# Kernel optimization log

Hardware: AMD Instinct MI355X
Metric: run time of the kernel (lower is better)

The kernel has to match this reference:

```python
import jax, jax.numpy as jnp
import numpy as np

B, N, H, F = 4, 256, 192, 64
SUP = 1.0  # ancestor_suppression_strength
EPS = 1e-6


def setup_inputs() -> dict:
    key = jax.random.key(0)
    ks = jax.random.split(key, 14)
    z = jax.random.normal(ks[0], (B, H), jnp.float32)
    # strictly-lower-triangular 0/1 parent (link) matrix: row t lists parents j < t
    tri = jnp.tril(jnp.ones((N, N), jnp.float32), -1)
    targets = (jax.random.uniform(ks[1], (B, N, N)) < 0.05).astype(jnp.float32) * tri

    def w(k, shape):
        fan_in = shape[0]
        return jax.random.normal(k, shape, jnp.float32) / jnp.sqrt(jnp.float32(fan_in))

    return {
        "z": z,
        "teacher_forcing_targets": targets,
        "W_init": w(ks[2], (H, H)), "b_init": jnp.zeros((H,), jnp.float32),
        "W_ih": w(ks[3], (H, 3 * H)), "W_hh": w(ks[4], (H, 3 * H)),
        "b_ih": jnp.zeros((3 * H,), jnp.float32), "b_hh": jnp.zeros((3 * H,), jnp.float32),
        "W1": w(ks[5], (3 * H, H)), "b1": jnp.zeros((H,), jnp.float32),
        "W2": w(ks[6], (H, 1)), "b2": jnp.zeros((1,), jnp.float32),
        "Wf": w(ks[7], (H, F)), "bf": jnp.zeros((F,), jnp.float32),
        "atom_count": N,
    }


def gru_cell(x, h, W_ih, W_hh, b_ih, b_hh):
    gx = x @ W_ih + b_ih
    gh = h @ W_hh + b_hh
    xr, xu, xn = jnp.split(gx, 3, axis=-1)
    hr, hu, hn = jnp.split(gh, 3, axis=-1)
    r = jax.nn.sigmoid(xr + hr)
    u = jax.nn.sigmoid(xu + hu)
    n = jnp.tanh(xn + r * hn)
    return (1.0 - u) * n + u * h


def reference(z, teacher_forcing_targets, W_init, b_init, W_ih, W_hh, b_ih, b_hh,
              W1, b1, W2, b2, Wf, bf, atom_count):
    b, n = teacher_forcing_targets.shape[0], teacher_forcing_targets.shape[1]
    h = z.shape[-1]
    idx = jnp.arange(n)

    # decoder_init: latent z -> hidden state of node 0
    h0 = jnp.tanh(z @ W_init + b_init)
    S0 = jnp.zeros((b, n, h), z.dtype).at[:, 0].set(h0)   # node states
    A0 = jnp.zeros((b, n, n), z.dtype)                    # ancestor indicator A[b,i,j]=1 iff j ancestor of i

    def step(carry, xs):
        S, A, ll = carry
        t, tgt = xs                                   # t scalar, tgt (B,N) = parents of node t
        mask = (idx < t).astype(S.dtype)              # existing nodes
        cnt = jnp.maximum(mask.sum(), 1.0)
        # mean-aggregation over existing node states -> GRU message
        m = (S * mask[None, :, None]).sum(axis=1) / cnt              # (B,H)
        h_prov = gru_cell(m, z, W_ih, W_hh, b_ih, b_hh)              # provisional state of new node
        # parent logits: MLP([h_new, h_existing, z]) per candidate parent
        feats = jnp.concatenate([
            jnp.broadcast_to(h_prov[:, None, :], S.shape), S,
            jnp.broadcast_to(z[:, None, :], S.shape)], axis=-1)      # (B,N,3H)
        logits = (jax.nn.relu(feats @ W1 + b1) @ W2 + b2)[..., 0]    # (B,N)
        # ancestor suppression: suppress j if j is already an ancestor of one of t's parents
        reach = jnp.einsum('bn,bnm->bm', tgt, A)
        anc = (reach > 0).astype(S.dtype)
        p = jax.nn.sigmoid(logits) * (1.0 - SUP * anc)
        p = jnp.clip(p, EPS, 1.0 - EPS)
        ll = ll + (mask[None, :] * (tgt * jnp.log(p) + (1.0 - tgt) * jnp.log1p(-p))).sum()
        # teacher forcing: commit parents, update new-node state from parent states
        deg = jnp.maximum(tgt.sum(axis=-1, keepdims=True), 1.0)
        msg = jnp.einsum('bn,bnh->bh', tgt, S) / deg
        h_new = gru_cell(msg, h_prov, W_ih, W_hh, b_ih, b_hh)
        S = jax.lax.dynamic_update_slice(S, h_new[:, None, :], (0, t, 0))
        row = jnp.minimum(tgt + anc, 1.0)             # ancestors(t) = parents U ancestors(parents)
        A = jax.lax.dynamic_update_slice(A, row[:, None, :], (0, t, 0))
        return (S, A, ll), None

    ts = jnp.arange(1, n)
    tgt_rows = jnp.swapaxes(teacher_forcing_targets[:, 1:, :], 0, 1)  # (N-1,B,N)
    (S, A, ll), _ = jax.lax.scan(step, (S0, A0, jnp.zeros((), z.dtype)), (ts, tgt_rows))

    L = teacher_forcing_targets            # teacher-forced link matrix
    node_features = S @ Wf + bf            # node_feature_decoder head
    return L, node_features, ll
```

## Files before the change

kernel.cpp:

```cpp
#include <hip/hip_runtime.h>
#include <stdint.h>

#define B_ 4
#define N_ 256
#define H_ 192
#define H3_ 576
#define F_ 64

#define H0_OFF   0u
#define ZC_OFF   1024u
#define HL_OFF   2048u
#define SL_OFF   395264u
#define AN_OFF   788480u
#define TG_OFF   796672u
#define PL_OFF   804864u
#define PC_OFF   870400u
#define DG_OFF   871424u
#define D_OFF    872448u
#define G_OFF    1462272u
#define C_OFF    1658880u
#define FHL_OFF  1855488u
#define FSL_OFF  2248704u
#define XC_OFF   2641920u

#define AN64 (AN_OFF/2)
#define TG64 (TG_OFF/2)

#define NF_OUT 262144u
#define LL_OUT 327680u

__device__ __forceinline__ float sigm_(float x){ return 1.0f/(1.0f + __expf(-x)); }
__device__ __forceinline__ float tanh_(float x){
  float ax = fabsf(x);
  float e = __expf(-2.0f*ax);
  float t = (1.0f - e)/(1.0f + e);
  return x < 0.0f ? -t : t;
}

__device__ __forceinline__ void st_mall_(uint32_t* p, unsigned long long u){
  __hip_atomic_store((unsigned long long*)p, u, __ATOMIC_RELAXED, __HIP_MEMORY_SCOPE_AGENT);
}
__device__ __forceinline__ unsigned long long ld_mall_(const uint32_t* p){
  return __hip_atomic_load((const unsigned long long*)p, __ATOMIC_RELAXED, __HIP_MEMORY_SCOPE_AGENT);
}
__device__ __forceinline__ unsigned long long ld_l2_(const uint32_t* p){
  unsigned long long v;
  asm volatile("buffer_inv sc0\n\t"
               "s_waitcnt vmcnt(0)\n\t"
               "global_load_dwordx2 %0, %1, off\n\t"
               "s_waitcnt vmcnt(0)"
               : "=v"(v) : "v"(p) : "memory");
  return v;
}
__device__ __forceinline__ void pub_(uint32_t* fp, uint32_t* mp, float v, uint32_t tag){
  unsigned long long u = ((unsigned long long)tag<<32) | (unsigned long long)__float_as_uint(v);
  __hip_atomic_store((unsigned long long*)fp, u, __ATOMIC_RELAXED, __HIP_MEMORY_SCOPE_WORKGROUP);
  st_mall_(mp, u);
}
__device__ __forceinline__ float pollH_(const uint32_t* fp, const uint32_t* mp, int fast, uint32_t tag){
  unsigned long long x = 0; int it = 0;
  for(;;){
    if (fast){
      x = ld_l2_(fp);
      if ((uint32_t)(x>>32) != tag && (((++it) & 3) == 3)){
        unsigned long long m = ld_mall_(mp);
        if ((uint32_t)(m>>32) == tag) x = m;
      }
    } else {
      x = ld_mall_(mp);
    }
    if (__all((int)((uint32_t)(x>>32) == tag))) break;
  }
  return __uint_as_float((uint32_t)x);
}

__global__ void __launch_bounds__(192) k_pre1(const float* __restrict__ z,
    const float* __restrict__ Winit, const float* __restrict__ binit,
    const float* __restrict__ W1, const float* __restrict__ b1,
    const float* __restrict__ tgt, float* ws, float* out)
{
  int bx = blockIdx.x, b = blockIdx.y, tid = threadIdx.x;
  if (bx == N_){
    __shared__ float zs[H_];
    zs[tid] = z[b*H_ + tid];
    __syncthreads();
    float a0=0.f, a1=0.f;
    for (int k=0;k<H_;k++){
      float zv = zs[k];
      a0 += zv * Winit[(size_t)k*H_ + tid];
      a1 += zv * W1[(size_t)(2*H_ + k)*H_ + tid];
    }
    ws[H0_OFF + b*H_ + tid] = tanh_(a0 + binit[tid]);
    ws[ZC_OFF + b*H_ + tid] = a1 + b1[tid];
    if (b==0 && tid==0) out[LL_OUT] = 0.0f;
    return;
  }
  if (tid >= 64) return;
  int t = bx, lane = tid;
  uint32_t* wsu = (uint32_t*)ws;
  unsigned long long* ws64 = (unsigned long long*)ws;
  const float* row = tgt + ((size_t)(b*N_) + t)*N_;
  uint8_t* pl = ((uint8_t*)&wsu[PL_OFF]) + (size_t)(b*N_ + t)*N_;
  int cnt = 0;
  #pragma unroll
  for (int m=0;m<4;m++){
    float v = row[m*64 + lane];
    bool p = (v != 0.0f);
    unsigned long long bw = __ballot(p);
    if (lane == 0) ws64[TG64 + (size_t)(b*N_+t)*4 + m] = bw;
    if (p){
      int pos = cnt + (int)__popcll(bw & ((1ULL<<lane)-1ULL));
      pl[pos] = (uint8_t)(m*64 + lane);
    }
    cnt += (int)__popcll(bw);
  }
  if (lane == 0){
    wsu[PC_OFF + b*N_ + t] = (uint32_t)cnt;
    ws[DG_OFF + b*N_ + t] = 1.0f / fmaxf((float)cnt, 1.0f);
  }
}

__global__ void __launch_bounds__(512, 2) k_pass1(const float* __restrict__ z,
    const float* __restrict__ Wih, const float* __restrict__ Whh,
    const float* __restrict__ bih_g, const float* __restrict__ bhh_g,
    float* ws)
{
  int bx = blockIdx.x;
  int b = bx & 7;
  if (b >= B_) return;
  int blk = bx >> 3;
  int tid = threadIdx.x;
  const int e  = tid >> 3;
  const int kc = tid & 7;
  const int E  = blk*64 + e;

  float* wsf = ws;
  uint32_t* wsu = (uint32_t*)ws;
  unsigned long long* ws64 = (unsigned long long*)ws;

  __shared__ __align__(16) float sh[H_];
  __shared__ __align__(16) float ss[H_];
  __shared__ float sDG[N_], sTF1[N_];
  __shared__ uint32_t sPC[N_];
  __shared__ int sfast[4];
  __shared__ unsigned long long sAB[N_][4];

  {
    float v = wsf[H0_OFF + b*H_ + E];
    if (kc == 0)
      pub_(&wsu[FSL_OFF + (unsigned)(b*N_)*384u + 2u*(unsigned)E],
           &wsu[SL_OFF  + (unsigned)(b*N_)*384u + 2u*(unsigned)E], v, 1u);
    if (kc == 1) ss[E] = v;
  }

  uint32_t xcc = (uint32_t)__builtin_amdgcn_s_getreg((31u<<11) | 20u) & 15u;
  if (tid == 0)
    __hip_atomic_store(&wsu[XC_OFF + b*16 + blk], 0xC0DE0000u | xcc,
                       __ATOMIC_RELAXED, __HIP_MEMORY_SCOPE_AGENT);
  if (tid < 64){
    uint32_t v = 0; int ok;
    do {
      v = (tid < 3) ? __hip_atomic_load(&wsu[XC_OFF + b*16 + tid],
              __ATOMIC_RELAXED, __HIP_MEMORY_SCOPE_AGENT) : (0xC0DE0000u | xcc);
      ok = (int)((v >> 16) == 0xC0DEu);
    } while (!__all(ok));
    if (tid < 3) sfast[tid] = ((v & 0xFFu) == xcc) ? 1 : 0;
  }

  for (int i = tid; i < N_; i += 512){
    sDG[i] = wsf[DG_OFF + b*N_ + i];
    sPC[i] = wsu[PC_OFF + b*N_ + i];
    float f1 = 0.f;
    if (i >= 1){
      unsigned long long w1 = ws64[TG64 + (size_t)(b*N_+i)*4 + ((i-1)>>6)];
      f1 = (float)((w1 >> ((i-1)&63)) & 1ULL);
    }
    sTF1[i] = f1;
  }
  if (blk == 0 && tid >= 192 && tid < 196) sAB[0][tid-192] = 0ULL;

  float rwih[3][24], rwhh[3][24], rbih[3], rbhh[3], rghz[3];
  #pragma unroll
  for (int g=0; g<3; g++){
    int col = g*H_ + E;
    #pragma unroll
    for (int i=0;i<24;i++){
      rwih[g][i] = Wih[(size_t)(kc*24+i)*H3_ + col];
      rwhh[g][i] = Whh[(size_t)(kc*24+i)*H3_ + col];
    }
    rbih[g] = bih_g[col];
    rbhh[g] = bhh_g[col];
  }
  {
    float a0=0.f,a1=0.f,a2=0.f;
    #pragma unroll
    for (int i=0;i<24;i++){
      float zv = z[b*H_ + kc*24 + i];
      a0 += zv*rwhh[0][i]; a1 += zv*rwhh[1][i]; a2 += zv*rwhh[2][i];
    }
    #pragma unroll
    for (int m=1;m<8;m<<=1){
      a0 += __shfl_xor(a0,m); a1 += __shfl_xor(a1,m); a2 += __shfl_xor(a2,m);
    }
    rghz[0]=a0+rbhh[0]; rghz[1]=a1+rbhh[1]; rghz[2]=a2+rbhh[2];
  }
  float zreg = z[b*H_ + E];

  __syncthreads();
  if (tid < 128){
    int j = (tid < blk*64) ? tid : tid + 64;
    ss[j] = pollH_(&wsu[FSL_OFF + (unsigned)(b*N_)*384u + 2u*(unsigned)j],
                   &wsu[SL_OFF  + (unsigned)(b*N_)*384u + 2u*(unsigned)j],
                   sfast[j>>6], 1u);
  }
  __syncthreads();

  float q0=0.f, q1=0.f, q2=0.f;
  const uint8_t* plbase = ((const uint8_t*)&wsu[PL_OFF]) + (size_t)(b*N_)*N_;
  float* Dbase = wsf + D_OFF + (size_t)((b*3+blk)*N_)*H_;

  for (int t=1; t<N_; t++){
    const uint32_t tagH = (uint32_t)(t+1);
    float d0=0.f,d1=0.f,d2=0.f;
    #pragma unroll
    for (int c=0;c<6;c++){
      float4 v4 = *(const float4*)&ss[kc*24 + c*4];
      float xx0=v4.x, xx1=v4.y, xx2=v4.z, xx3=v4.w;
      d0 += xx0*rwih[0][c*4+0]; d1 += xx0*rwih[1][c*4+0]; d2 += xx0*rwih[2][c*4+0];
      d0 += xx1*rwih[0][c*4+1]; d1 += xx1*rwih[1][c*4+1]; d2 += xx1*rwih[2][c*4+1];
      d0 += xx2*rwih[0][c*4+2]; d1 += xx2*rwih[1][c*4+2]; d2 += xx2*rwih[2][c*4+2];
      d0 += xx3*rwih[0][c*4+3]; d1 += xx3*rwih[1][c*4+3]; d2 += xx3*rwih[2][c*4+3];
    }
    #pragma unroll
    for (int m=1;m<8;m<<=1){
      d0 += __shfl_xor(d0,m); d1 += __shfl_xor(d1,m); d2 += __shfl_xor(d2,m);
    }
    q0 += d0; q1 += d1; q2 += d2;
    float invt = 1.0f/(float)t;
    float r = sigm_(q0*invt + rbih[0] + rghz[0]);
    float u = sigm_(q1*invt + rbih[1] + rghz[1]);
    float n = tanh_(q2*invt + rbih[2] + r*rghz[2]);
    float hp = (1.0f-u)*n + u*zreg;
    if (kc == 0){
      pub_(&wsu[FHL_OFF + (unsigned)(b*N_+t)*384u + 2u*(unsigned)E],
           &wsu[HL_OFF  + (unsigned)(b*N_+t)*384u + 2u*(unsigned)E], hp, tagH);
      float* Dr = Dbase + (size_t)(t-1)*H_;
      Dr[e] = d0; Dr[64+e] = d1; Dr[128+e] = d2;
    }
    if (kc == 1) sh[E] = hp;
    float ga0=0.f, ga1=0.f, ga2=0.f;
    {
      int pc = (int)sPC[t];
      const uint8_t* pl = plbase + (size_t)t*N_;
      for (int i=kc; i<pc; i+=8){
        int p = pl[i];
        if (p == t-1) continue;
        const float* Dp = Dbase + (size_t)p*H_;
        ga0 += Dp[e]; ga1 += Dp[64+e]; ga2 += Dp[128+e];
      }
    }
    #pragma unroll
    for (int m=1;m<8;m<<=1){
      ga0 += __shfl_xor(ga0,m); ga1 += __shfl_xor(ga1,m); ga2 += __shfl_xor(ga2,m);
    }
    if (tid < 128){
      int j = (tid < blk*64) ? tid : tid + 64;
      sh[j] = pollH_(&wsu[FHL_OFF + (unsigned)(b*N_+t)*384u + 2u*(unsigned)j],
                     &wsu[HL_OFF  + (unsigned)(b*N_+t)*384u + 2u*(unsigned)j],
                     sfast[j>>6], tagH);
    } else if (blk == 0 && tid >= 192 && tid < 208){
      int lane16 = tid - 192;
      int ip = lane16 >> 2, w = lane16 & 3;
      int pc = (int)sPC[t];
      const uint8_t* pl = plbase + (size_t)t*N_;
      unsigned long long acc = 0ULL;
      for (int i=ip; i<pc; i+=4) acc |= sAB[pl[i]][w];
      acc |= __shfl_xor(acc, 4);
      acc |= __shfl_xor(acc, 8);
      if (ip == 0){
        ws64[AN64 + (size_t)(b*N_+t)*4 + w] = acc;
        sAB[t][w] = acc | ws64[TG64 + (size_t)(b*N_+t)*4 + w];
      }
    }
    __syncthreads();
    float y0=0.f,y1=0.f,y2=0.f;
    #pragma unroll
    for (int c=0;c<6;c++){
      float4 v4 = *(const float4*)&sh[kc*24 + c*4];
      float xx0=v4.x, xx1=v4.y, xx2=v4.z, xx3=v4.w;
      y0 += xx0*rwhh[0][c*4+0]; y1 += xx0*rwhh[1][c*4+0]; y2 += xx0*rwhh[2][c*4+0];
      y0 += xx1*rwhh[0][c*4+1]; y1 += xx1*rwhh[1][c*4+1]; y2 += xx1*rwhh[2][c*4+1];
      y0 += xx2*rwhh[0][c*4+2]; y1 += xx2*rwhh[1][c*4+2]; y2 += xx2*rwhh[2][c*4+2];
      y0 += xx3*rwhh[0][c*4+3]; y1 += xx3*rwhh[1][c*4+3]; y2 += xx3*rwhh[2][c*4+3];
    }
    #pragma unroll
    for (int m=1;m<8;m<<=1){
      y0 += __shfl_xor(y0,m); y1 += __shfl_xor(y1,m); y2 += __shfl_xor(y2,m);
    }
    float dginv = sDG[t], tf1 = sTF1[t];
    float gxa = (ga0 + tf1*d0)*dginv + rbih[0];
    float gxb = (ga1 + tf1*d1)*dginv + rbih[1];
    float gxc = (ga2 + tf1*d2)*dginv + rbih[2];
    float r2 = sigm_(gxa + y0 + rbhh[0]);
    float u2 = sigm_(gxb + y1 + rbhh[1]);
    float n2 = tanh_(gxc + r2*(y2 + rbhh[2]));
    float hn = (1.0f-u2)*n2 + u2*hp;
    if (kc == 0)
      pub_(&wsu[FSL_OFF + (unsigned)(b*N_+t)*384u + 2u*(unsigned)E],
           &wsu[SL_OFF  + (unsigned)(b*N_+t)*384u + 2u*(unsigned)E], hn, tagH);
    if (kc == 1) ss[E] = hn;
    if (tid < 128){
      int j = (tid < blk*64) ? tid : tid + 64;
      ss[j] = pollH_(&wsu[FSL_OFF + (unsigned)(b*N_+t)*384u + 2u*(unsigned)j],
                     &wsu[SL_OFF  + (unsigned)(b*N_+t)*384u + 2u*(unsigned)j],
                     sfast[j>>6], tagH);
    }
    __syncthreads();
  }
}

__global__ void k_p2a(const float* __restrict__ W1, const float* __restrict__ Wf,
    const float* __restrict__ bf, float* ws, float* out)
{
  int j = blockIdx.x, b = blockIdx.y, tid = threadIdx.x;
  __shared__ float srow[H_], hrow[H_];
  __shared__ float nfp[3][F_];
  srow[tid] = ws[SL_OFF + (unsigned)(b*N_+j)*384u + 2u*tid];
  hrow[tid] = ws[HL_OFF + (unsigned)(b*N_+j)*384u + 2u*tid];
  __syncthreads();
  float accG = 0.f, accC = 0.f;
  for (int k=0;k<H_;k++){
    float sv = srow[k], hv = hrow[k];
    accG += sv * W1[(size_t)(H_+k)*H_ + tid];
    accC += hv * W1[(size_t)k*H_ + tid];
  }
  ws[G_OFF + ((size_t)b*H_ + tid)*N_ + j] = accG;
  ws[C_OFF + (size_t)(b*N_+j)*H_ + tid] = accC + ws[ZC_OFF + b*H_ + tid];
  int f = tid & 63, kp = tid >> 6;
  float a = 0.f;
  for (int i=0;i<64;i++){ int k = kp*64 + i; a += srow[k]*Wf[(size_t)k*F_ + f]; }
  nfp[kp][f] = a;
  __syncthreads();
  if (tid < F_) out[NF_OUT + (size_t)(b*N_+j)*F_ + tid] = nfp[0][tid]+nfp[1][tid]+nfp[2][tid] + bf[tid];
}

__global__ void __launch_bounds__(256) k_p2b(const float* __restrict__ W2,
    const float* __restrict__ b2p, float* ws, float* out)
{
  int t = blockIdx.x + 1, b = blockIdx.y;
  int tid = threadIdx.x; int lane = tid & 63; int wv = tid >> 6;
  __shared__ float cv[H_], w2s[H_];
  __shared__ float wsum[4];
  unsigned long long* ws64 = (unsigned long long*)ws;
  if (tid < H_){
    cv[tid] = ws[C_OFF + (size_t)(b*N_+t)*H_ + tid];
    w2s[tid] = W2[tid];
  }
  __syncthreads();
  float acc = 0.f;
  if (tid < t){
    const float* GT = ws + G_OFF + (size_t)b*H_*N_;
    float a = 0.f;
    for (int k=0;k<H_;k++) a += fmaxf(cv[k] + GT[(size_t)k*N_ + tid], 0.f) * w2s[k];
    float logit = a + b2p[0];
    float pp = 1.0f/(1.0f+__expf(-logit));
    unsigned long long an = ws64[AN64 + (size_t)(b*N_+t)*4 + (tid>>6)];
    unsigned long long tg = ws64[TG64 + (size_t)(b*N_+t)*4 + (tid>>6)];
    float anc = (float)((an >> (tid&63)) & 1ULL);
    pp = pp * (1.0f - anc);
    pp = fminf(fmaxf(pp, 1e-6f), 1.0f - 1e-6f);
    int tgb = (int)((tg >> (tid&63)) & 1ULL);
    acc = tgb ? logf(pp) : log1pf(-pp);
  }
  #pragma unroll
  for (int m=32;m>=1;m>>=1) acc += __shfl_xor(acc, m);
  if (lane == 0) wsum[wv] = acc;
  __syncthreads();
  if (tid == 0) atomicAdd(out + LL_OUT, wsum[0]+wsum[1]+wsum[2]+wsum[3]);
}

extern "C" void kernel_launch(void* const* d_in, const int* in_sizes, int n_in,
                              void* d_out, int out_size, void* d_ws, size_t ws_size,
                              hipStream_t stream) {
  (void)in_sizes; (void)n_in; (void)out_size; (void)ws_size;
  const float* z     = (const float*)d_in[0];
  const float* tgt   = (const float*)d_in[1];
  const float* Winit = (const float*)d_in[2];
  const float* binit = (const float*)d_in[3];
  const float* Wih   = (const float*)d_in[4];
  const float* Whh   = (const float*)d_in[5];
  const float* bih   = (const float*)d_in[6];
  const float* bhh   = (const float*)d_in[7];
  const float* W1    = (const float*)d_in[8];
  const float* b1    = (const float*)d_in[9];
  const float* W2    = (const float*)d_in[10];
  const float* b2    = (const float*)d_in[11];
  const float* Wf    = (const float*)d_in[12];
  const float* bf    = (const float*)d_in[13];
  float* out = (float*)d_out;
  float* ws  = (float*)d_ws;

  hipMemcpyAsync(d_out, d_in[1], (size_t)B_*N_*N_*sizeof(float), hipMemcpyDeviceToDevice, stream);

  k_pre1<<<dim3(N_+1, B_), dim3(192), 0, stream>>>(z, Winit, binit, W1, b1, tgt, ws, out);
  k_pass1<<<dim3(24), dim3(512), 0, stream>>>(z, Wih, Whh, bih, bhh, ws);
  k_p2a<<<dim3(N_, B_), dim3(H_), 0, stream>>>(W1, Wf, bf, ws, out);
  k_p2b<<<dim3(N_-1, B_), dim3(256), 0, stream>>>(W2, b2, ws, out);
}
```

Before: 938.0 us.

## Offload MALL mirror stores to idle waves and use lighter barrier

```diff
diff --git a/kernel.cpp b/kernel.cpp
--- a/kernel.cpp
+++ b/kernel.cpp
@@ -52,10 +52,21 @@
                : "=v"(v) : "v"(p) : "memory");
   return v;
 }
-__device__ __forceinline__ void pub_(uint32_t* fp, uint32_t* mp, float v, uint32_t tag){
+__device__ __forceinline__ void pubF_(uint32_t* fp, float v, uint32_t tag){
+  unsigned long long u = ((unsigned long long)tag<<32) | (unsigned long long)__float_as_uint(v);
+  __hip_atomic_store((unsigned long long*)fp, u, __ATOMIC_RELAXED, __HIP_MEMORY_SCOPE_WORKGROUP);
+}
+__device__ __forceinline__ void pub2_(uint32_t* fp, uint32_t* mp, float v, uint32_t tag){
   unsigned long long u = ((unsigned long long)tag<<32) | (unsigned long long)__float_as_uint(v);
   __hip_atomic_store((unsigned long long*)fp, u, __ATOMIC_RELAXED, __HIP_MEMORY_SCOPE_WORKGROUP);
   st_mall_(mp, u);
+}
+__device__ __forceinline__ void mirror_(const uint32_t* fp, uint32_t* mp, uint32_t tag){
+  unsigned long long x;
+  do {
+    x = __hip_atomic_load((const unsigned long long*)fp, __ATOMIC_RELAXED, __HIP_MEMORY_SCOPE_WORKGROUP);
+  } while ((uint32_t)(x>>32) != tag);
+  st_mall_(mp, x);
 }
 __device__ __forceinline__ float pollH_(const uint32_t* fp, const uint32_t* mp, int fast, uint32_t tag){
   unsigned long long x = 0; int it = 0;
@@ -72,6 +83,11 @@
     if (__all((int)((uint32_t)(x>>32) == tag))) break;
   }
   return __uint_as_float((uint32_t)x);
+}
+__device__ __forceinline__ void bar_(){
+  asm volatile("s_waitcnt lgkmcnt(0)" ::: "memory");
+  __builtin_amdgcn_s_barrier();
+  asm volatile("" ::: "memory");
 }
 
 __global__ void __launch_bounds__(192) k_pre1(const float* __restrict__ z,
@@ -120,7 +136,7 @@
   }
 }
 
-__global__ void __launch_bounds__(512, 2) k_pass1(const float* __restrict__ z,
+__global__ void __launch_bounds__(512, 1) k_pass1(const float* __restrict__ z,
     const float* __restrict__ Wih, const float* __restrict__ Whh,
     const float* __restrict__ bih_g, const float* __restrict__ bhh_g,
     float* ws)
@@ -148,8 +164,8 @@
   {
     float v = wsf[H0_OFF + b*H_ + E];
     if (kc == 0)
-      pub_(&wsu[FSL_OFF + (unsigned)(b*N_)*384u + 2u*(unsigned)E],
-           &wsu[SL_OFF  + (unsigned)(b*N_)*384u + 2u*(unsigned)E], v, 1u);
+      pub2_(&wsu[FSL_OFF + (unsigned)(b*N_)*384u + 2u*(unsigned)E],
+            &wsu[SL_OFF  + (unsigned)(b*N_)*384u + 2u*(unsigned)E], v, 1u);
     if (kc == 1) ss[E] = v;
   }
 
@@ -242,8 +258,7 @@
     float n = tanh_(q2*invt + rbih[2] + r*rghz[2]);
     float hp = (1.0f-u)*n + u*zreg;
     if (kc == 0){
-      pub_(&wsu[FHL_OFF + (unsigned)(b*N_+t)*384u + 2u*(unsigned)E],
-           &wsu[HL_OFF  + (unsigned)(b*N_+t)*384u + 2u*(unsigned)E], hp, tagH);
+      pubF_(&wsu[FHL_OFF + (unsigned)(b*N_+t)*384u + 2u*(unsigned)E], hp, tagH);
       float* Dr = Dbase + (size_t)(t-1)*H_;
       Dr[e] = d0; Dr[64+e] = d1; Dr[128+e] = d2;
     }
@@ -268,7 +283,12 @@
       sh[j] = pollH_(&wsu[FHL_OFF + (unsigned)(b*N_+t)*384u + 2u*(unsigned)j],
                      &wsu[HL_OFF  + (unsigned)(b*N_+t)*384u + 2u*(unsigned)j],
                      sfast[j>>6], tagH);
-    } else if (blk == 0 && tid >= 192 && tid < 208){
+    } else if (tid < 192){
+      int ml = tid - 128;
+      unsigned em = (unsigned)(blk*64 + ml);
+      mirror_(&wsu[FHL_OFF + (unsigned)(b*N_+t)*384u + 2u*em],
+              &wsu[HL_OFF  + (unsigned)(b*N_+t)*384u + 2u*em], tagH);
+    } else if (blk == 0 && tid < 208){
       int lane16 = tid - 192;
       int ip = lane16 >> 2, w = lane16 & 3;
       int pc = (int)sPC[t];
@@ -282,7 +302,7 @@
         sAB[t][w] = acc | ws64[TG64 + (size_t)(b*N_+t)*4 + w];
       }
     }
-    __syncthreads();
+    bar_();
     float y0=0.f,y1=0.f,y2=0.f;
     #pragma unroll
     for (int c=0;c<6;c++){
@@ -306,16 +326,20 @@
     float n2 = tanh_(gxc + r2*(y2 + rbhh[2]));
     float hn = (1.0f-u2)*n2 + u2*hp;
     if (kc == 0)
-      pub_(&wsu[FSL_OFF + (unsigned)(b*N_+t)*384u + 2u*(unsigned)E],
-           &wsu[SL_OFF  + (unsigned)(b*N_+t)*384u + 2u*(unsigned)E], hn, tagH);
+      pubF_(&wsu[FSL_OFF + (unsigned)(b*N_+t)*384u + 2u*(unsigned)E], hn, tagH);
     if (kc == 1) ss[E] = hn;
     if (tid < 128){
       int j = (tid < blk*64) ? tid : tid + 64;
       ss[j] = pollH_(&wsu[FSL_OFF + (unsigned)(b*N_+t)*384u + 2u*(unsigned)j],
                      &wsu[SL_OFF  + (unsigned)(b*N_+t)*384u + 2u*(unsigned)j],
                      sfast[j>>6], tagH);
-    }
-    __syncthreads();
+    } else if (tid >= 192 && tid < 256){
+      int ml = tid - 192;
+      unsigned em = (unsigned)(blk*64 + ml);
+      mirror_(&wsu[FSL_OFF + (unsigned)(b*N_+t)*384u + 2u*em],
+              &wsu[SL_OFF  + (unsigned)(b*N_+t)*384u + 2u*em], tagH);
+    }
+    bar_();
   }
 }
 
```

New measurement: 1.069 ms. 1.14x slower.
